# Optimization experiments

Hardware: AMD Instinct MI355X
Metric: run time of the kernel (lower is better)

## Reference

```python
import jax, jax.numpy as jnp
import numpy as np

N = 50000      # nodes
E = 800000     # edges (before self loops)
F_IN = 50      # PPI num_features
H = 4          # heads
C = 64         # hidden per head
NC = 121       # PPI num_classes
NEG_SLOPE = 0.2


def setup_inputs() -> dict:
    key = jax.random.key(0)
    ks = jax.random.split(key, 20)
    p = lambda k, shape: (jax.random.normal(k, shape, jnp.float32) * 0.1)
    x0 = jax.random.normal(ks[0], (N, F_IN), jnp.float32)
    edge_index = jax.random.randint(ks[1], (2, E), 0, N, dtype=jnp.int64)
    return dict(
        x0=x0, edge_index=edge_index,
        W1=p(ks[2], (F_IN, H * C)), as1=p(ks[3], (H, C)), ad1=p(ks[4], (H, C)),
        res1=p(ks[5], (F_IN, H * C)), b1=jnp.zeros((H * C,), jnp.float32),
        W2=p(ks[6], (H * C, H * C)), as2=p(ks[7], (H, C)), ad2=p(ks[8], (H, C)),
        res2=p(ks[9], (H * C, H * C)), b2=jnp.zeros((H * C,), jnp.float32),
        W3=p(ks[10], (H * C, H * NC)), as3=p(ks[11], (H, NC)), ad3=p(ks[12], (H, NC)),
        res3=p(ks[13], (H * C, NC)), b3=jnp.zeros((NC,), jnp.float32),
    )


def _gat(x, src, dst, W, a_src, a_dst, resW, b, concat):
    """PyG-style GATConv with residual, self loops already in (src, dst)."""
    n = x.shape[0]
    heads, outc = a_src.shape
    h = (x @ W).reshape(n, heads, outc)                 # [N,H,C]
    al_s = (h * a_src).sum(-1)                          # [N,H]
    al_d = (h * a_dst).sum(-1)                          # [N,H]
    e = jax.nn.leaky_relu(al_s[src] + al_d[dst], NEG_SLOPE)  # [E,H]
    m = jax.ops.segment_max(e, dst, num_segments=n)     # stable softmax per dst
    ex = jnp.exp(e - m[dst])
    denom = jax.ops.segment_sum(ex, dst, num_segments=n)
    alpha = ex / denom[dst]                             # [E,H]
    out = jax.ops.segment_sum(h[src] * alpha[:, :, None], dst, num_segments=n)  # [N,H,C]
    out = out.reshape(n, heads * outc) if concat else out.mean(axis=1)
    return out + x @ resW + b


def reference(x0, edge_index,
              W1, as1, ad1, res1, b1,
              W2, as2, ad2, res2, b2,
              W3, as3, ad3, res3, b3):
    n = x0.shape[0]
    loop = jnp.arange(n, dtype=edge_index.dtype)        # add self loops (PyG default)
    src = jnp.concatenate([edge_index[0], loop])
    dst = jnp.concatenate([edge_index[1], loop])
    x1 = jax.nn.relu(_gat(x0, src, dst, W1, as1, ad1, res1, b1, True))
    x2 = jax.nn.relu(_gat(x1, src, dst, W2, as2, ad2, res2, b2, True))
    x3 = _gat(x2, src, dst, W3, as3, ad3, res3, b3, False)
    return x3
```

## Files before the change

### kernel.cpp

```cpp
#include <hip/hip_runtime.h>

#define NNODES 50000
#define NEDGES 800000
#define NTOT   (NEDGES + NNODES)
#define F_IN   50
#define KPAD1  64
#define HEADS  4
#define C1     64
#define HC1    256
#define NC     121
#define K1S    320
#define K3S    1280
#define N2S    512

typedef unsigned short ushort_t;
typedef __attribute__((ext_vector_type(4))) unsigned short ushort4_t;
typedef __attribute__((ext_vector_type(8))) unsigned short ushort8;
typedef __attribute__((ext_vector_type(8))) __bf16 bf16x8;
typedef __attribute__((ext_vector_type(4))) float f32x4;

__device__ __forceinline__ ushort_t f2bf(float f) {
    union { float f; unsigned int u; } v; v.f = f;
    unsigned int u = v.u;
    return (ushort_t)((u + 0x7fffu + ((u >> 16) & 1u)) >> 16);
}
__device__ __forceinline__ float bf2f(ushort_t s) {
    union { unsigned int u; float f; } v; v.u = ((unsigned int)s) << 16;
    return v.f;
}
__device__ __forceinline__ f32x4 bf4_to_f32x4(ushort4_t v) {
    union { ushort4_t u4; unsigned int d[2]; } u; u.u4 = v;
    union { unsigned int u; float f; } c0, c1, c2, c3;
    c0.u = u.d[0] << 16; c1.u = u.d[0] & 0xffff0000u;
    c2.u = u.d[1] << 16; c3.u = u.d[1] & 0xffff0000u;
    f32x4 r; r.x = c0.f; r.y = c1.f; r.z = c2.f; r.w = c3.f;
    return r;
}
__device__ __forceinline__ float lrelu(float x) { return x > 0.f ? x : 0.2f * x; }

__global__ void count_kernel(const int* __restrict__ ei, int* __restrict__ cnt) {
    int i = blockIdx.x * blockDim.x + threadIdx.x;
    if (i >= NTOT) return;
    int d = (i < NEDGES) ? ei[NEDGES + i] : (i - NEDGES);
    if ((unsigned)d >= NNODES) d = 0;
    atomicAdd(&cnt[d], 1);
}

#define SCB 256
__global__ __launch_bounds__(SCB)
void scan1_kernel(const int* __restrict__ cnt, int* __restrict__ incl,
                  int* __restrict__ bsums, int n) {
    __shared__ int buf[SCB];
    int b = blockIdx.x, tid = threadIdx.x;
    int i = b * SCB + tid;
    int v = (i < n) ? cnt[i] : 0;
    buf[tid] = v;
    __syncthreads();
    for (int off = 1; off < SCB; off <<= 1) {
        int t = (tid >= off) ? buf[tid - off] : 0;
        __syncthreads();
        buf[tid] += t;
        __syncthreads();
    }
    if (i < n) incl[i] = buf[tid];
    if (tid == SCB - 1) bsums[b] = buf[tid];
}

__global__ __launch_bounds__(SCB)
void scan2_kernel(int* __restrict__ bsums, int nb) {
    __shared__ int buf[SCB];
    int tid = threadIdx.x;
    int v = (tid < nb) ? bsums[tid] : 0;
    buf[tid] = v;
    __syncthreads();
    for (int off = 1; off < SCB; off <<= 1) {
        int t = (tid >= off) ? buf[tid - off] : 0;
        __syncthreads();
        buf[tid] += t;
        __syncthreads();
    }
    if (tid < nb) bsums[tid] = buf[tid] - v;
}

__global__ __launch_bounds__(SCB)
void scan3_kernel(const int* __restrict__ cnt, const int* __restrict__ incl,
                  const int* __restrict__ bsums, int* __restrict__ row_ptr,
                  int* __restrict__ cursor, int n) {
    int b = blockIdx.x, tid = threadIdx.x;
    int i = b * SCB + tid;
    if (i >= n) return;
    int e = bsums[b] + incl[i] - cnt[i];
    row_ptr[i] = e; cursor[i] = e;
    if (i == n - 1) row_ptr[n] = NTOT;
}

__global__ void scatter_kernel(const int* __restrict__ ei, int* __restrict__ cursor,
                               int* __restrict__ csr_src) {
    int i = blockIdx.x * blockDim.x + threadIdx.x;
    if (i >= NTOT) return;
    int s, d;
    if (i < NEDGES) { s = ei[i]; d = ei[NEDGES + i]; }
    else            { s = d = i - NEDGES; }
    if ((unsigned)d >= NNODES) d = 0;
    if ((unsigned)s >= NNODES) s = 0;
    int pos = atomicAdd(&cursor[d], 1);
    csr_src[pos] = s;
}

#define SZ_A (NNODES * KPAD1)
#define SZ_B (HC1 * K1S)
#define SZ_C (N2S * HC1)
#define SZ_D (N2S)
#define SZ_E (NC * K3S)
#define SZ_F (KPAD1 * 4)
#define SZ_G (HC1 * 4)
#define PREP_TOTAL (SZ_A + SZ_B + SZ_C + SZ_D + SZ_E + 2 * SZ_F + 4 * SZ_G)

__global__ __launch_bounds__(256)
void prep_kernel(const float* __restrict__ x0,
                 const float* __restrict__ W1, const float* __restrict__ res1,
                 const float* __restrict__ W2, const float* __restrict__ res2,
                 const float* __restrict__ W3, const float* __restrict__ res3,
                 const float* __restrict__ as1, const float* __restrict__ ad1,
                 const float* __restrict__ as2, const float* __restrict__ ad2,
                 const float* __restrict__ as3, const float* __restrict__ ad3,
                 const float* __restrict__ b2,
                 ushort_t* __restrict__ x0b, ushort_t* __restrict__ Bt1,
                 ushort_t* __restrict__ Bt2, ushort_t* __restrict__ Bt3,
                 float* __restrict__ bias512,
                 float* __restrict__ w_as1, float* __restrict__ w_ad1,
                 float* __restrict__ w_as2, float* __restrict__ w_ad2,
                 float* __restrict__ w_as3, float* __restrict__ w_ad3) {
    int i = blockIdx.x * 256 + threadIdx.x;
    if (i < SZ_A) {
        int m = i >> 6, k = i & 63;
        x0b[i] = (k < F_IN) ? f2bf(x0[(size_t)m * F_IN + k]) : (ushort_t)0;
        return;
    }
    i -= SZ_A;
    if (i < SZ_B) {
        int c = i / K1S, kk = i - c * K1S;
        float v = 0.f;
        if (kk < 256) {
            int h = kk >> 6, k = kk & 63;
            if (k < F_IN && (c >> 6) == h) v = W1[(size_t)k * HC1 + c];
        } else {
            int k = kk - 256;
            if (k < F_IN) v = res1[(size_t)k * HC1 + c];
        }
        Bt1[i] = f2bf(v);
        return;
    }
    i -= SZ_B;
    if (i < SZ_C) {
        int c = i / HC1, k = i - c * HC1;
        float v = (c < HC1) ? W2[(size_t)k * HC1 + c] : res2[(size_t)k * HC1 + (c - HC1)];
        Bt2[i] = f2bf(v);
        return;
    }
    i -= SZ_C;
    if (i < SZ_D) {
        bias512[i] = (i < HC1) ? 0.f : b2[i - HC1];
        return;
    }
    i -= SZ_D;
    if (i < SZ_E) {
        int c = i / K3S, kk = i - c * K3S;
        float v;
        if (kk < 1024) {
            int h = kk >> 8, k = kk & 255;
            v = 0.25f * W3[(size_t)k * (HEADS * NC) + h * NC + c];
        } else {
            int k = kk - 1024;
            v = res3[(size_t)k * NC + c];
        }
        Bt3[i] = f2bf(v);
        return;
    }
    i -= SZ_E;
    if (i < 2 * SZ_F) {
        const float* a = (i < SZ_F) ? as1 : ad1;
        float* w = (i < SZ_F) ? w_as1 : w_ad1;
        int ii = (i < SZ_F) ? i : i - SZ_F;
        int k = ii >> 2, h = ii & 3;
        float s = 0.f;
        if (k < F_IN)
            for (int c = 0; c < C1; ++c) s += W1[(size_t)k * HC1 + h * C1 + c] * a[h * C1 + c];
        w[ii] = s;
        return;
    }
    i -= 2 * SZ_F;
    {
        int grp = i / SZ_G, ii = i - grp * SZ_G;
        int k = ii >> 2, h = ii & 3;
        float s = 0.f;
        if (grp < 2) {
            const float* a = grp ? ad2 : as2;
            for (int c = 0; c < C1; ++c) s += W2[(size_t)k * HC1 + h * C1 + c] * a[h * C1 + c];
            (grp ? w_ad2 : w_as2)[ii] = s;
        } else {
            const float* a = (grp == 3) ? ad3 : as3;
            for (int c = 0; c < NC; ++c) s += W3[(size_t)k * (HEADS * NC) + h * NC + c] * a[h * NC + c];
            ((grp == 3) ? w_ad3 : w_as3)[ii] = s;
        }
    }
}

#define BM 128
#define BN 128
#define BK 64
#define LDP (BK + 8)

__global__ __launch_bounds__(256)
void gemm_mfma_kernel(const ushort_t* __restrict__ A1, int lda1,
                      const ushort_t* __restrict__ A2, int lda2, int Ksplit,
                      const ushort_t* __restrict__ Bt, const float* __restrict__ bias,
                      float* __restrict__ Cf, ushort_t* __restrict__ Cb,
                      int M, int N, int K, int relu) {
    __shared__ ushort_t As[BM * LDP];
    __shared__ ushort_t Bs[BN * LDP];
    int tid = threadIdx.x;
    int lane = tid & 63;
    int wid = tid >> 6;
    int wm = (wid & 1) * 64, wn = (wid >> 1) * 64;
    int l15 = lane & 15;
    int q8 = (lane >> 4) * 8;
    int m0 = blockIdx.y * BM, n0 = blockIdx.x * BN;

    f32x4 acc[4][4] = {};

    for (int k0 = 0; k0 < K; k0 += BK) {
        #pragma unroll
        for (int it = 0; it < 4; ++it) {
            int c = tid + it * 256;
            int row = c >> 3, c8 = c & 7;
            int k = k0 + c8 * 8;
            ushort8 va = (ushort8)0;
            int gm = m0 + row;
            if (gm < M) {
                if (k < Ksplit) va = *(const ushort8*)&A1[(size_t)gm * lda1 + k];
                else            va = *(const ushort8*)&A2[(size_t)gm * lda2 + (k - Ksplit)];
            }
            *(ushort8*)&As[row * LDP + c8 * 8] = va;
            ushort8 vb = (ushort8)0;
            int gn = n0 + row;
            if (gn < N) vb = *(const ushort8*)&Bt[(size_t)gn * K + k];
            *(ushort8*)&Bs[row * LDP + c8 * 8] = vb;
        }
        __syncthreads();
        #pragma unroll
        for (int kk = 0; kk < BK; kk += 32) {
            bf16x8 af[4], bfr[4];
            #pragma unroll
            for (int mi = 0; mi < 4; ++mi)
                af[mi] = *(const bf16x8*)&As[(wm + mi * 16 + l15) * LDP + kk + q8];
            #pragma unroll
            for (int ni = 0; ni < 4; ++ni)
                bfr[ni] = *(const bf16x8*)&Bs[(wn + ni * 16 + l15) * LDP + kk + q8];
            #pragma unroll
            for (int mi = 0; mi < 4; ++mi)
                #pragma unroll
                for (int ni = 0; ni < 4; ++ni)
                    acc[mi][ni] = __builtin_amdgcn_mfma_f32_16x16x32_bf16(
                        af[mi], bfr[ni], acc[mi][ni], 0, 0, 0);
        }
        __syncthreads();
    }

    #pragma unroll
    for (int mi = 0; mi < 4; ++mi) {
        int mbase = m0 + wm + mi * 16 + (lane >> 4) * 4;
        #pragma unroll
        for (int ni = 0; ni < 4; ++ni) {
            int ncol = n0 + wn + ni * 16 + l15;
            if (ncol >= N) continue;
            float bv = bias ? bias[ncol] : 0.f;
            #pragma unroll
            for (int r = 0; r < 4; ++r) {
                int m = mbase + r;
                if (m >= M) continue;
                float v = acc[mi][ni][r] + bv;
                if (relu) v = fmaxf(v, 0.f);
                if (Cf) Cf[(size_t)m * N + ncol] = v;
                else    Cb[(size_t)m * N + ncol] = f2bf(v);
            }
        }
    }
}

__global__ __launch_bounds__(64)
void logits_gemv_kernel(const ushort_t* __restrict__ X, int K,
                        const float* __restrict__ w_as, const float* __restrict__ w_ad,
                        float* __restrict__ als, float* __restrict__ ald) {
    int n = blockIdx.x, lane = threadIdx.x;
    float ps[HEADS] = {}, pd[HEADS] = {};
    for (int k0 = lane * 4; k0 < K; k0 += 256) {
        ushort4_t xv = *(const ushort4_t*)&X[(size_t)n * K + k0];
        float x[4] = {bf2f(xv.x), bf2f(xv.y), bf2f(xv.z), bf2f(xv.w)};
        #pragma unroll
        for (int j = 0; j < 4; ++j) {
            #pragma unroll
            for (int h = 0; h < HEADS; ++h) {
                ps[h] += x[j] * w_as[(k0 + j) * 4 + h];
                pd[h] += x[j] * w_ad[(k0 + j) * 4 + h];
            }
        }
    }
    #pragma unroll
    for (int off = 32; off; off >>= 1)
        #pragma unroll
        for (int h = 0; h < HEADS; ++h) {
            ps[h] += __shfl_xor(ps[h], off);
            pd[h] += __shfl_xor(pd[h], off);
        }
    if (lane == 0)
        #pragma unroll
        for (int h = 0; h < HEADS; ++h) {
            als[n * HEADS + h] = ps[h];
            ald[n * HEADS + h] = pd[h];
        }
}

#define MAX_PASS(als_, ald_)                                                  \
    int beg = row_ptr[d], end = row_ptr[d + 1];                               \
    f32x4 aldd = *(const f32x4*)&(ald_)[d * 4];                               \
    float mx[HEADS] = {-1e30f, -1e30f, -1e30f, -1e30f};                       \
    for (int i = beg + lane; i < end; i += 64) {                              \
        f32x4 av = *(const f32x4*)&(als_)[csr_src[i] * 4];                    \
        _Pragma("unroll")                                                     \
        for (int h = 0; h < HEADS; ++h)                                       \
            mx[h] = fmaxf(mx[h], lrelu(av[h] + aldd[h]));                     \
    }                                                                         \
    _Pragma("unroll")                                                         \
    for (int off = 32; off; off >>= 1)                                        \
        _Pragma("unroll")                                                     \
        for (int h = 0; h < HEADS; ++h)                                       \
            mx[h] = fmaxf(mx[h], __shfl_xor(mx[h], off));

#define E_CHUNK(als_)                                                         \
    int i = base + lane;                                                      \
    int nv = end - base; if (nv > 64) nv = 64;                                \
    if (i < end) {                                                            \
        int s = csr_src[i];                                                   \
        ssrc[lane] = s;                                                       \
        f32x4 av = *(const f32x4*)&(als_)[s * 4];                             \
        f32x4 e;                                                              \
        _Pragma("unroll")                                                     \
        for (int h = 0; h < HEADS; ++h) {                                     \
            e[h] = __expf(lrelu(av[h] + aldd[h]) - mx[h]);                    \
            den[h] += e[h];                                                   \
        }                                                                     \
        *(f32x4*)&se[lane * 4] = e;                                           \
    }                                                                         \
    __syncthreads();

#define DEN_REDUCE                                                            \
    _Pragma("unroll")                                                         \
    for (int off = 32; off; off >>= 1)                                        \
        _Pragma("unroll")                                                     \
        for (int h = 0; h < HEADS; ++h)                                       \
            den[h] += __shfl_xor(den[h], off);                                \
    float rd[HEADS];                                                          \
    _Pragma("unroll")                                                         \
    for (int h = 0; h < HEADS; ++h) rd[h] = 1.f / den[h];

__global__ __launch_bounds__(64)
void agg1_kernel(const ushort_t* __restrict__ x0b,
                 const float* __restrict__ als, const float* __restrict__ ald,
                 const int* __restrict__ row_ptr, const int* __restrict__ csr_src,
                 ushort_t* __restrict__ aggx) {
    __shared__ int   ssrc[64];
    __shared__ float se[64 * 4];
    int d = blockIdx.x, lane = threadIdx.x;
    MAX_PASS(als, ald)
    float den[HEADS] = {};
    f32x4 acc = (f32x4)0.f;
    for (int base = beg; base < end; base += 64) {
        E_CHUNK(als)
        int j = 0;
        for (; j + 4 <= nv; j += 4) {
            int s0 = ssrc[j], s1 = ssrc[j + 1], s2 = ssrc[j + 2], s3 = ssrc[j + 3];
            f32x4 e0 = *(const f32x4*)&se[j * 4];
            f32x4 e1 = *(const f32x4*)&se[(j + 1) * 4];
            f32x4 e2 = *(const f32x4*)&se[(j + 2) * 4];
            f32x4 e3 = *(const f32x4*)&se[(j + 3) * 4];
            float x0v = bf2f(x0b[(size_t)s0 * KPAD1 + lane]);
            float x1v = bf2f(x0b[(size_t)s1 * KPAD1 + lane]);
            float x2v = bf2f(x0b[(size_t)s2 * KPAD1 + lane]);
            float x3v = bf2f(x0b[(size_t)s3 * KPAD1 + lane]);
            acc += e0 * x0v + e1 * x1v + e2 * x2v + e3 * x3v;
        }
        for (; j < nv; ++j) {
            f32x4 e = *(const f32x4*)&se[j * 4];
            acc += e * bf2f(x0b[(size_t)ssrc[j] * KPAD1 + lane]);
        }
        __syncthreads();
    }
    DEN_REDUCE
    #pragma unroll
    for (int h = 0; h < HEADS; ++h)
        aggx[(size_t)d * HC1 + h * 64 + lane] = f2bf(acc[h] * rd[h]);
}

__global__ __launch_bounds__(64)
void agg2_kernel(const ushort_t* __restrict__ comb,
                 const float* __restrict__ als, const float* __restrict__ ald,
                 const int* __restrict__ row_ptr, const int* __restrict__ csr_src,
                 const float* __restrict__ w_as3, const float* __restrict__ w_ad3,
                 ushort_t* __restrict__ xnext,
                 float* __restrict__ als3, float* __restrict__ ald3) {
    __shared__ int   ssrc[64];
    __shared__ float se[64 * 4];
    int d = blockIdx.x, lane = threadIdx.x;
    int hh = lane >> 4;
    MAX_PASS(als, ald)
    float den[HEADS] = {};
    f32x4 acc = (f32x4)0.f;
    for (int base = beg; base < end; base += 64) {
        E_CHUNK(als)
        int j = 0;
        for (; j + 8 <= nv; j += 8) {
            int s0 = ssrc[j],     s1 = ssrc[j + 1], s2 = ssrc[j + 2], s3 = ssrc[j + 3];
            int s4 = ssrc[j + 4], s5 = ssrc[j + 5], s6 = ssrc[j + 6], s7 = ssrc[j + 7];
            float e0 = se[j * 4 + hh],       e1 = se[(j + 1) * 4 + hh];
            float e2 = se[(j + 2) * 4 + hh], e3 = se[(j + 3) * 4 + hh];
            float e4 = se[(j + 4) * 4 + hh], e5 = se[(j + 5) * 4 + hh];
            float e6 = se[(j + 6) * 4 + hh], e7 = se[(j + 7) * 4 + hh];
            f32x4 x0 = bf4_to_f32x4(*(const ushort4_t*)&comb[(size_t)s0 * N2S + lane * 4]);
            f32x4 x1 = bf4_to_f32x4(*(const ushort4_t*)&comb[(size_t)s1 * N2S + lane * 4]);
            f32x4 x2 = bf4_to_f32x4(*(const ushort4_t*)&comb[(size_t)s2 * N2S + lane * 4]);
            f32x4 x3 = bf4_to_f32x4(*(const ushort4_t*)&comb[(size_t)s3 * N2S + lane * 4]);
            f32x4 x4 = bf4_to_f32x4(*(const ushort4_t*)&comb[(size_t)s4 * N2S + lane * 4]);
            f32x4 x5 = bf4_to_f32x4(*(const ushort4_t*)&comb[(size_t)s5 * N2S + lane * 4]);
            f32x4 x6 = bf4_to_f32x4(*(const ushort4_t*)&comb[(size_t)s6 * N2S + lane * 4]);
            f32x4 x7 = bf4_to_f32x4(*(const ushort4_t*)&comb[(size_t)s7 * N2S + lane * 4]);
            acc += e0 * x0 + e1 * x1 + e2 * x2 + e3 * x3
                 + e4 * x4 + e5 * x5 + e6 * x6 + e7 * x7;
        }
        for (; j < nv; ++j) {
            float e = se[j * 4 + hh];
            f32x4 xv = bf4_to_f32x4(*(const ushort4_t*)&comb[(size_t)ssrc[j] * N2S + lane * 4]);
            acc += e * xv;
        }
        __syncthreads();
    }
    DEN_REDUCE
    float r = rd[hh];
    f32x4 rv = bf4_to_f32x4(*(const ushort4_t*)&comb[(size_t)d * N2S + 256 + lane * 4]);
    float v0 = fmaxf(acc.x * r + rv.x, 0.f);
    float v1 = fmaxf(acc.y * r + rv.y, 0.f);
    float v2 = fmaxf(acc.z * r + rv.z, 0.f);
    float v3 = fmaxf(acc.w * r + rv.w, 0.f);
    ushort4_t o;
    o.x = f2bf(v0); o.y = f2bf(v1); o.z = f2bf(v2); o.w = f2bf(v3);
    *(ushort4_t*)&xnext[(size_t)d * HC1 + lane * 4] = o;
    f32x4 ps = (f32x4)0.f, pd = (f32x4)0.f;
    float v[4] = {v0, v1, v2, v3};
    #pragma unroll
    for (int j = 0; j < 4; ++j) {
        f32x4 wsj = *(const f32x4*)&w_as3[(lane * 4 + j) * 4];
        f32x4 wdj = *(const f32x4*)&w_ad3[(lane * 4 + j) * 4];
        ps += v[j] * wsj;
        pd += v[j] * wdj;
    }
    #pragma unroll
    for (int off = 32; off; off >>= 1) {
        #pragma unroll
        for (int h = 0; h < HEADS; ++h) {
            ps[h] += __shfl_xor(ps[h], off);
            pd[h] += __shfl_xor(pd[h], off);
        }
    }
    if (lane == 0) {
        *(f32x4*)&als3[d * 4] = ps;
        *(f32x4*)&ald3[d * 4] = pd;
    }
}

__global__ __launch_bounds__(64)
void agg3_kernel(const ushort_t* __restrict__ x2b,
                 const float* __restrict__ als, const float* __restrict__ ald,
                 const int* __restrict__ row_ptr, const int* __restrict__ csr_src,
                 ushort_t* __restrict__ aggx) {
    __shared__ int   ssrc[64];
    __shared__ float se[64 * 4];
    int d = blockIdx.x, lane = threadIdx.x;
    MAX_PASS(als, ald)
    float den[HEADS] = {};
    f32x4 acc[HEADS] = {};
    for (int base = beg; base < end; base += 64) {
        E_CHUNK(als)
        int j = 0;
        for (; j + 4 <= nv; j += 4) {
            int s0 = ssrc[j], s1 = ssrc[j + 1], s2 = ssrc[j + 2], s3 = ssrc[j + 3];
            f32x4 e0 = *(const f32x4*)&se[j * 4];
            f32x4 e1 = *(const f32x4*)&se[(j + 1) * 4];
            f32x4 e2 = *(const f32x4*)&se[(j + 2) * 4];
            f32x4 e3 = *(const f32x4*)&se[(j + 3) * 4];
            f32x4 x0 = bf4_to_f32x4(*(const ushort4_t*)&x2b[(size_t)s0 * HC1 + lane * 4]);
            f32x4 x1 = bf4_to_f32x4(*(const ushort4_t*)&x2b[(size_t)s1 * HC1 + lane * 4]);
            f32x4 x2 = bf4_to_f32x4(*(const ushort4_t*)&x2b[(size_t)s2 * HC1 + lane * 4]);
            f32x4 x3 = bf4_to_f32x4(*(const ushort4_t*)&x2b[(size_t)s3 * HC1 + lane * 4]);
            #pragma unroll
            for (int h = 0; h < HEADS; ++h)
                acc[h] += e0[h] * x0 + e1[h] * x1 + e2[h] * x2 + e3[h] * x3;
        }
        for (; j < nv; ++j) {
            f32x4 e = *(const f32x4*)&se[j * 4];
            f32x4 xv = bf4_to_f32x4(*(const ushort4_t*)&x2b[(size_t)ssrc[j] * HC1 + lane * 4]);
            #pragma unroll
            for (int h = 0; h < HEADS; ++h) acc[h] += e[h] * xv;
        }
        __syncthreads();
    }
    DEN_REDUCE
    #pragma unroll
    for (int h = 0; h < HEADS; ++h) {
        ushort4_t o;
        o.x = f2bf(acc[h].x * rd[h]); o.y = f2bf(acc[h].y * rd[h]);
        o.z = f2bf(acc[h].z * rd[h]); o.w = f2bf(acc[h].w * rd[h]);
        *(ushort4_t*)&aggx[(size_t)d * 1024 + h * HC1 + lane * 4] = o;
    }
}

extern "C" void kernel_launch(void* const* d_in, const int* in_sizes, int n_in,
                              void* d_out, int out_size, void* d_ws, size_t ws_size,
                              hipStream_t stream) {
    const float* x0   = (const float*)d_in[0];
    const int*   ei   = (const int*)d_in[1];
    const float* W1   = (const float*)d_in[2];
    const float* as1  = (const float*)d_in[3];
    const float* ad1  = (const float*)d_in[4];
    const float* res1 = (const float*)d_in[5];
    const float* b1   = (const float*)d_in[6];
    const float* W2   = (const float*)d_in[7];
    const float* as2  = (const float*)d_in[8];
    const float* ad2  = (const float*)d_in[9];
    const float* res2 = (const float*)d_in[10];
    const float* b2   = (const float*)d_in[11];
    const float* W3   = (const float*)d_in[12];
    const float* as3  = (const float*)d_in[13];
    const float* ad3  = (const float*)d_in[14];
    const float* res3 = (const float*)d_in[15];
    const float* b3   = (const float*)d_in[16];

    char* p = (char*)d_ws;
    auto alloc = [&](size_t bytes) -> void* {
        void* r = (void*)p;
        p += (bytes + 255) & ~(size_t)255;
        return r;
    };
    int*      cnt     = (int*)alloc((size_t)NNODES * 4);
    int*      incl    = (int*)alloc((size_t)NNODES * 4);
    int*      bsums   = (int*)alloc((size_t)SCB * 4);
    int*      row_ptr = (int*)alloc((size_t)(NNODES + 1) * 4);
    int*      cursor  = (int*)alloc((size_t)NNODES * 4);
    int*      csr_src = (int*)alloc((size_t)NTOT * 4);
    float*    als     = (float*)alloc((size_t)NNODES * HEADS * 4);
    float*    ald     = (float*)alloc((size_t)NNODES * HEADS * 4);
    float*    als3    = (float*)alloc((size_t)NNODES * HEADS * 4);
    float*    ald3    = (float*)alloc((size_t)NNODES * HEADS * 4);
    ushort_t* x0b     = (ushort_t*)alloc((size_t)NNODES * KPAD1 * 2);
    ushort_t* x2      = (ushort_t*)alloc((size_t)NNODES * HC1 * 2);
    ushort_t* Bt1     = (ushort_t*)alloc((size_t)HC1 * K1S * 2);
    ushort_t* Bt2     = (ushort_t*)alloc((size_t)N2S * HC1 * 2);
    float*    bias512 = (float*)alloc((size_t)N2S * 4);
    ushort_t* Bt3     = (ushort_t*)alloc((size_t)NC * K3S * 2);
    float*    w_as1   = (float*)alloc((size_t)KPAD1 * 4 * 4);
    float*    w_ad1   = (float*)alloc((size_t)KPAD1 * 4 * 4);
    float*    w_as2   = (float*)alloc((size_t)HC1 * 4 * 4);
    float*    w_ad2   = (float*)alloc((size_t)HC1 * 4 * 4);
    float*    w_as3   = (float*)alloc((size_t)HC1 * 4 * 4);
    float*    w_ad3   = (float*)alloc((size_t)HC1 * 4 * 4);
    char*     big     = (char*)alloc((size_t)NNODES * 1024 * 2);
    ushort_t* aggx1   = (ushort_t*)big;
    ushort_t* x1      = (ushort_t*)(big + (size_t)NNODES * HC1 * 2);
    ushort_t* comb    = (ushort_t*)(big + (size_t)NNODES * HC1 * 4);
    ushort_t* aggx3   = (ushort_t*)big;

    hipMemsetAsync(cnt, 0, (size_t)NNODES * 4, stream);

    int tb = 256;
    int nscan = (NNODES + SCB - 1) / SCB;
    count_kernel<<<(NTOT + tb - 1) / tb, tb, 0, stream>>>(ei, cnt);
    scan1_kernel<<<nscan, SCB, 0, stream>>>(cnt, incl, bsums, NNODES);
    scan2_kernel<<<1, SCB, 0, stream>>>(bsums, nscan);
    scan3_kernel<<<nscan, SCB, 0, stream>>>(cnt, incl, bsums, row_ptr, cursor, NNODES);
    scatter_kernel<<<(NTOT + tb - 1) / tb, tb, 0, stream>>>(ei, cursor, csr_src);

    prep_kernel<<<(PREP_TOTAL + 255) / 256, 256, 0, stream>>>(
        x0, W1, res1, W2, res2, W3, res3, as1, ad1, as2, ad2, as3, ad3, b2,
        x0b, Bt1, Bt2, Bt3, bias512, w_as1, w_ad1, w_as2, w_ad2, w_as3, w_ad3);

    auto gemm = [&](const ushort_t* A1, int lda1, const ushort_t* A2, int lda2, int Ksplit,
                    const ushort_t* Bt, const float* bias,
                    float* Cf, ushort_t* Cb, int M, int Nn, int K, int relu) {
        dim3 g((Nn + BN - 1) / BN, (M + BM - 1) / BM);
        gemm_mfma_kernel<<<g, 256, 0, stream>>>(A1, lda1, A2, lda2, Ksplit, Bt, bias,
                                                Cf, Cb, M, Nn, K, relu);
    };

    logits_gemv_kernel<<<NNODES, 64, 0, stream>>>(x0b, KPAD1, w_as1, w_ad1, als, ald);
    agg1_kernel<<<NNODES, 64, 0, stream>>>(x0b, als, ald, row_ptr, csr_src, aggx1);
    gemm(aggx1, HC1, x0b, KPAD1, HC1, Bt1, b1, nullptr, x1, NNODES, HC1, K1S, 1);

    gemm(x1, HC1, x1, HC1, HC1, Bt2, bias512, nullptr, comb, NNODES, N2S, HC1, 0);
    logits_gemv_kernel<<<NNODES, 64, 0, stream>>>(x1, HC1, w_as2, w_ad2, als, ald);
    agg2_kernel<<<NNODES, 64, 0, stream>>>(comb, als, ald, row_ptr, csr_src,
                                           w_as3, w_ad3, x2, als3, ald3);

    agg3_kernel<<<NNODES, 64, 0, stream>>>(x2, als3, ald3, row_ptr, csr_src, aggx3);
    gemm(aggx3, 1024, x2, HC1, 1024, Bt3, b3, (float*)d_out, nullptr, NNODES, NC, K3S, 0);
}
```

Baseline: 655.3 us.

## Fuse degree count into prep kernel, unroll agg3 by 8, nontemporal stores

```diff
diff --git a/kernel.cpp b/kernel.cpp
--- a/kernel.cpp
+++ b/kernel.cpp
@@ -38,14 +38,6 @@
 }
 __device__ __forceinline__ float lrelu(float x) { return x > 0.f ? x : 0.2f * x; }
 
-__global__ void count_kernel(const int* __restrict__ ei, int* __restrict__ cnt) {
-    int i = blockIdx.x * blockDim.x + threadIdx.x;
-    if (i >= NTOT) return;
-    int d = (i < NEDGES) ? ei[NEDGES + i] : (i - NEDGES);
-    if ((unsigned)d >= NNODES) d = 0;
-    atomicAdd(&cnt[d], 1);
-}
-
 #define SCB 256
 __global__ __launch_bounds__(SCB)
 void scan1_kernel(const int* __restrict__ cnt, int* __restrict__ incl,
@@ -114,10 +106,11 @@
 #define SZ_E (NC * K3S)
 #define SZ_F (KPAD1 * 4)
 #define SZ_G (HC1 * 4)
-#define PREP_TOTAL (SZ_A + SZ_B + SZ_C + SZ_D + SZ_E + 2 * SZ_F + 4 * SZ_G)
+#define PREP_TOTAL (NTOT + SZ_A + SZ_B + SZ_C + SZ_D + SZ_E + 2 * SZ_F + 4 * SZ_G)
 
 __global__ __launch_bounds__(256)
-void prep_kernel(const float* __restrict__ x0,
+void prep_kernel(const int* __restrict__ ei, int* __restrict__ cnt,
+                 const float* __restrict__ x0,
                  const float* __restrict__ W1, const float* __restrict__ res1,
                  const float* __restrict__ W2, const float* __restrict__ res2,
                  const float* __restrict__ W3, const float* __restrict__ res3,
@@ -132,6 +125,13 @@
                  float* __restrict__ w_as2, float* __restrict__ w_ad2,
                  float* __restrict__ w_as3, float* __restrict__ w_ad3) {
     int i = blockIdx.x * 256 + threadIdx.x;
+    if (i < NTOT) {
+        int d = (i < NEDGES) ? ei[NEDGES + i] : (i - NEDGES);
+        if ((unsigned)d >= NNODES) d = 0;
+        atomicAdd(&cnt[d], 1);
+        return;
+    }
+    i -= NTOT;
     if (i < SZ_A) {
         int m = i >> 6, k = i & 63;
         x0b[i] = (k < F_IN) ? f2bf(x0[(size_t)m * F_IN + k]) : (ushort_t)0;
@@ -399,7 +399,8 @@
     DEN_REDUCE
     #pragma unroll
     for (int h = 0; h < HEADS; ++h)
-        aggx[(size_t)d * HC1 + h * 64 + lane] = f2bf(acc[h] * rd[h]);
+        __builtin_nontemporal_store(f2bf(acc[h] * rd[h]),
+                                    &aggx[(size_t)d * HC1 + h * 64 + lane]);
 }
 
 __global__ __launch_bounds__(64)
@@ -491,6 +492,30 @@
     for (int base = beg; base < end; base += 64) {
         E_CHUNK(als)
         int j = 0;
+        for (; j + 8 <= nv; j += 8) {
+            int s0 = ssrc[j],     s1 = ssrc[j + 1], s2 = ssrc[j + 2], s3 = ssrc[j + 3];
+            int s4 = ssrc[j + 4], s5 = ssrc[j + 5], s6 = ssrc[j + 6], s7 = ssrc[j + 7];
+            f32x4 e0 = *(const f32x4*)&se[j * 4];
+            f32x4 e1 = *(const f32x4*)&se[(j + 1) * 4];
+            f32x4 e2 = *(const f32x4*)&se[(j + 2) * 4];
+            f32x4 e3 = *(const f32x4*)&se[(j + 3) * 4];
+            f32x4 e4 = *(const f32x4*)&se[(j + 4) * 4];
+            f32x4 e5 = *(const f32x4*)&se[(j + 5) * 4];
+            f32x4 e6 = *(const f32x4*)&se[(j + 6) * 4];
+            f32x4 e7 = *(const f32x4*)&se[(j + 7) * 4];
+            f32x4 x0 = bf4_to_f32x4(*(const ushort4_t*)&x2b[(size_t)s0 * HC1 + lane * 4]);
+            f32x4 x1 = bf4_to_f32x4(*(const ushort4_t*)&x2b[(size_t)s1 * HC1 + lane * 4]);
+            f32x4 x2 = bf4_to_f32x4(*(const ushort4_t*)&x2b[(size_t)s2 * HC1 + lane * 4]);
+            f32x4 x3 = bf4_to_f32x4(*(const ushort4_t*)&x2b[(size_t)s3 * HC1 + lane * 4]);
+            f32x4 x4 = bf4_to_f32x4(*(const ushort4_t*)&x2b[(size_t)s4 * HC1 + lane * 4]);
+            f32x4 x5 = bf4_to_f32x4(*(const ushort4_t*)&x2b[(size_t)s5 * HC1 + lane * 4]);
+            f32x4 x6 = bf4_to_f32x4(*(const ushort4_t*)&x2b[(size_t)s6 * HC1 + lane * 4]);
+            f32x4 x7 = bf4_to_f32x4(*(const ushort4_t*)&x2b[(size_t)s7 * HC1 + lane * 4]);
+            #pragma unroll
+            for (int h = 0; h < HEADS; ++h)
+                acc[h] += e0[h] * x0 + e1[h] * x1 + e2[h] * x2 + e3[h] * x3
+                        + e4[h] * x4 + e5[h] * x5 + e6[h] * x6 + e7[h] * x7;
+        }
         for (; j + 4 <= nv; j += 4) {
             int s0 = ssrc[j], s1 = ssrc[j + 1], s2 = ssrc[j + 2], s3 = ssrc[j + 3];
             f32x4 e0 = *(const f32x4*)&se[j * 4];
@@ -519,7 +544,7 @@
         ushort4_t o;
         o.x = f2bf(acc[h].x * rd[h]); o.y = f2bf(acc[h].y * rd[h]);
         o.z = f2bf(acc[h].z * rd[h]); o.w = f2bf(acc[h].w * rd[h]);
-        *(ushort4_t*)&aggx[(size_t)d * 1024 + h * HC1 + lane * 4] = o;
+        __builtin_nontemporal_store(o, (ushort4_t*)&aggx[(size_t)d * 1024 + h * HC1 + lane * 4]);
     }
 }
 
@@ -582,15 +607,15 @@
 
     int tb = 256;
     int nscan = (NNODES + SCB - 1) / SCB;
-    count_kernel<<<(NTOT + tb - 1) / tb, tb, 0, stream>>>(ei, cnt);
+
+    prep_kernel<<<(PREP_TOTAL + 255) / 256, 256, 0, stream>>>(
+        ei, cnt, x0, W1, res1, W2, res2, W3, res3, as1, ad1, as2, ad2, as3, ad3, b2,
+        x0b, Bt1, Bt2, Bt3, bias512, w_as1, w_ad1, w_as2, w_ad2, w_as3, w_ad3);
+
     scan1_kernel<<<nscan, SCB, 0, stream>>>(cnt, incl, bsums, NNODES);
     scan2_kernel<<<1, SCB, 0, stream>>>(bsums, nscan);
     scan3_kernel<<<nscan, SCB, 0, stream>>>(cnt, incl, bsums, row_ptr, cursor, NNODES);
     scatter_kernel<<<(NTOT + tb - 1) / tb, tb, 0, stream>>>(ei, cursor, csr_src);
-
-    prep_kernel<<<(PREP_TOTAL + 255) / 256, 256, 0, stream>>>(
-        x0, W1, res1, W2, res2, W3, res3, as1, ad1, as2, ad2, as3, ad3, b2,
-        x0b, Bt1, Bt2, Bt3, bias512, w_as1, w_ad1, w_as2, w_ad2, w_as3, w_ad3);
 
     auto gemm = [&](const ushort_t* A1, int lda1, const ushort_t* A2, int lda2, int Ksplit,
                     const ushort_t* Bt, const float* bias,
```

Result: no change. 667.8 us (+1.9%).
